# Performance work log

Hardware: AMD Instinct MI355X
Metric: run time of the kernel (lower is better)

## Reference

```python
import jax, jax.numpy as jnp
import numpy as np

K = 3; PAD = 1; STRIDE = 1; EPS = 1e-5


def setup_inputs() -> dict:
    key = jax.random.key(0)
    k0, k1, k2 = jax.random.split(key, 3)
    B, C, H, W, O = 4, 256, 64, 64, 256
    x = jax.random.normal(k0, (B, C, H, W), jnp.float32)
    # offset conv: small random weights so offsets are nontrivial but bounded
    w_off = jax.random.normal(k1, (2 * K * K, C, K, K), jnp.float32) * 0.01
    b_off = jnp.zeros((2 * K * K,), jnp.float32)
    # kaiming normal, mode=fan_out: std = sqrt(2 / (O*K*K))
    w_def = jax.random.normal(k2, (O, C, K, K), jnp.float32) * np.float32(np.sqrt(2.0 / (O * K * K)))
    gamma = jnp.ones((O,), jnp.float32)
    beta = jnp.zeros((O,), jnp.float32)
    return {"x": x, "w_off": w_off, "b_off": b_off, "w_def": w_def, "gamma": gamma, "beta": beta}


def _bilinear_gather(x, py, px):
    """x: [B,C,H,W]; py,px: [B,K2,Ho,Wo] float sample coords.
    Returns [B,K2,Ho,Wo,C] with zero padding outside (per-corner masking,
    matching torchvision deform_conv2d)."""
    B, C, H, W = x.shape
    y0f = jnp.floor(py); x0f = jnp.floor(px)
    wy1 = py - y0f; wy0 = 1.0 - wy1
    wx1 = px - x0f; wx0 = 1.0 - wx1
    bidx = jnp.arange(B)[:, None, None, None]

    def corner(yf, xf, wgt):
        valid = (yf >= 0) & (yf <= H - 1) & (xf >= 0) & (xf <= W - 1)
        yc = jnp.clip(yf.astype(jnp.int32), 0, H - 1)
        xc = jnp.clip(xf.astype(jnp.int32), 0, W - 1)
        v = x[bidx, :, yc, xc]  # [B,K2,Ho,Wo,C] (advanced idx moves C last)
        return v * (wgt * valid)[..., None]

    return (corner(y0f, x0f, wy0 * wx0) + corner(y0f, x0f + 1.0, wy0 * wx1)
            + corner(y0f + 1.0, x0f, wy1 * wx0) + corner(y0f + 1.0, x0f + 1.0, wy1 * wx1))


def _forward(x, w_off, b_off, w_def, gamma, beta):
    B, C, H, W = x.shape
    O = w_def.shape[0]
    K2 = K * K
    # 1) offset-predicting conv
    off = jax.lax.conv_general_dilated(x, w_off, (STRIDE, STRIDE), ((PAD, PAD), (PAD, PAD)))
    off = off + b_off[None, :, None, None]
    Ho, Wo = off.shape[2], off.shape[3]
    off = off.reshape(B, K2, 2, Ho, Wo)  # pairs (dy, dx) per kernel tap
    # 2) deformable sampling locations
    ky, kx = jnp.meshgrid(jnp.arange(K, dtype=jnp.float32), jnp.arange(K, dtype=jnp.float32), indexing='ij')
    base_y = (jnp.arange(Ho, dtype=jnp.float32) * STRIDE - PAD)
    base_x = (jnp.arange(Wo, dtype=jnp.float32) * STRIDE - PAD)
    py = off[:, :, 0] + ky.reshape(K2)[None, :, None, None] + base_y[None, None, :, None]
    px = off[:, :, 1] + kx.reshape(K2)[None, :, None, None] + base_x[None, None, None, :]
    vals = _bilinear_gather(x, py, px)  # [B,K2,Ho,Wo,C]
    # 3) deform conv GEMM (bias=False)
    out = jnp.einsum('bkhwc,ock->bohw', vals, w_def.reshape(O, C, K2))
    # 4) BatchNorm (training mode: batch stats) + ReLU
    mean = out.mean(axis=(0, 2, 3))
    var = out.var(axis=(0, 2, 3))
    out = (out - mean[None, :, None, None]) * (gamma * jax.lax.rsqrt(var + EPS))[None, :, None, None]
    out = out + beta[None, :, None, None]
    return jax.nn.relu(out)


def reference(x, w_off, b_off, w_def, gamma, beta):
    return _forward(x, w_off, b_off, w_def, gamma, beta)
```

## Files before the change

### kernel.cpp

```cpp
#include <hip/hip_runtime.h>
#include <hip/hip_bf16.h>

typedef unsigned int  uint;
typedef unsigned short ushort;
typedef short bf16x8 __attribute__((ext_vector_type(8)));
typedef float f32x4  __attribute__((ext_vector_type(4)));

#define HW   4096
#define KD   2304

__device__ __forceinline__ void load_lds16(const void* g, void* l) {
    __builtin_amdgcn_global_load_lds((const __attribute__((address_space(1))) void*)g,
                                     (__attribute__((address_space(3))) void*)l, 16, 0, 0);
}
__device__ __forceinline__ float blo(uint u) { return __uint_as_float(u << 16); }
__device__ __forceinline__ float bhi(uint u) { return __uint_as_float(u & 0xffff0000u); }
__device__ __forceinline__ uint pack2(float e, float o) {
    __hip_bfloat16 he = __float2bfloat16(e), ho = __float2bfloat16(o);
    return (uint)(*(ushort*)&he) | ((uint)(*(ushort*)&ho) << 16);
}

__global__ __launch_bounds__(256) void prep_all(const float* __restrict__ x,
                                                const float* __restrict__ w_def,
                                                const float* __restrict__ w_off,
                                                uint* __restrict__ x2t,
                                                ushort* __restrict__ bt,
                                                ushort* __restrict__ bt0,
                                                float* __restrict__ stats) {
    __shared__ uint tl[32][65];
    int bid = blockIdx.x;
    int t = threadIdx.x;
    if (bid < 1024) {
        int ab  = bid & 63;
        int cpb = (bid >> 6) & 3;
        int b   = bid >> 8;
#pragma unroll
        for (int i = 0; i < 8; ++i) {
            int idx = i * 256 + t;
            int cp = idx >> 6, a = idx & 63;
            const float* p = x + ((size_t)(b * 256 + (cpb * 32 + cp) * 2)) * HW + ab * 64 + a;
            tl[cp][a] = pack2(p[0], p[HW]);
        }
        __syncthreads();
#pragma unroll
        for (int i = 0; i < 8; ++i) {
            int idx = i * 256 + t;
            int a = idx >> 5, cp = idx & 31;
            x2t[((size_t)b * 4096 + ab * 64 + a) * 128 + cpb * 32 + cp] = tl[cp][a];
        }
    } else if (bid < 3328) {
        int idx = (bid - 1024) * 256 + t;
        int c   = idx & 255;
        int tap = (idx >> 8) % 9;
        int o   = idx / KD;
        __hip_bfloat16 h = __float2bfloat16(w_def[(o * 256 + c) * 9 + tap]);
        bt[idx] = *(ushort*)&h;
    } else if (bid < 3616) {
        int idx = (bid - 3328) * 256 + t;
        int c   = idx & 255;
        int tap = (idx >> 8) % 9;
        int j   = idx / KD;
        float v = (j < 18) ? w_off[(j * 256 + c) * 9 + tap] : 0.f;
        __hip_bfloat16 h = __float2bfloat16(v);
        bt0[idx] = *(ushort*)&h;
    } else {
        float4 z = {0.f, 0.f, 0.f, 0.f};
        ((float4*)stats)[t] = z;
    }
}

__global__ __attribute__((amdgpu_waves_per_eu(4, 4))) __launch_bounds__(1024)
void fused_main(const uint* __restrict__ x2t,
                const ushort* __restrict__ bt,
                const ushort* __restrict__ bt0,
                const float* __restrict__ b_off,
                float* __restrict__ out,
                float* __restrict__ stats) {
    int id = blockIdx.x;
    int xcd = id & 7;
    int b = xcd >> 1, h = (xcd & 1) * 32 + (id >> 3);
    int t = threadIdx.x;
    int wv = t >> 6, lane = t & 63;
    int mrow = lane & 15, quad = lane >> 4;
    bool producer = (wv < 8);
    int ppos = (wv << 3) + (lane >> 3);
    int pc8  = lane & 7;
    int wvc  = wv - 8;

    __shared__ __align__(16) char smem[66048];
    uint*   lX   = (uint*)smem;
    ushort* lB0  = (ushort*)(smem + 24576);
    float*  sOff = (float*)(smem + 61440);
    int*    sAc  = (int*)smem;
    float*  sWc  = (float*)(smem + 9216);
    ushort* lA   = (ushort*)(smem + 18432);

    {
        f32x4 accO = {0.f, 0.f, 0.f, 0.f};
        int mq = wv & 3, nn = (wv >> 2) & 1;
        for (int cb = 0; cb < 4; ++cb) {
#pragma unroll
            for (int s = 0; s < 2; ++s) {
                int q = s * 16 + wv;
                if (q < 24) {
                    int dy  = q >> 3;
                    int y   = h + dy - 1;
                    int sub = q & 7;
                    int wl  = sub * 8 + (lane >> 3);
                    int cps = ((lane & 7) ^ ((lane >> 3) & 7)) * 4;
                    if ((unsigned)y < 64u) {
                        const uint* src = x2t + ((size_t)(b * 4096 + y * 64 + wl)) * 128 + cb * 32 + cps;
                        load_lds16(src, &lX[q * 256]);
                    } else {
                        uint4 z = {0u, 0u, 0u, 0u};
                        *(uint4*)&lX[q * 256 + lane * 4] = z;
                    }
                }
            }
#pragma unroll
            for (int s = 0; s < 3; ++s) {
                int q = s * 16 + wv;
                if (q < 36) {
                    int e = q * 512 + lane * 8;
                    int o  = e / 576;
                    int r  = e - o * 576;
                    int chp = r >> 3;
                    int ch  = chp ^ (o & 7);
                    int tap = ch >> 3, k8 = ch & 7;
                    const ushort* src = bt0 + (size_t)o * KD + tap * 256 + cb * 64 + k8 * 8;
                    load_lds16(src, &lB0[q * 512]);
                }
            }
            __syncthreads();
            if (producer) {
#pragma unroll
                for (int tap = 0; tap < 9; ++tap) {
                    int dy = tap / 3, dx = tap % 3;
                    int xx = mq * 16 + mrow + dx - 1;
                    bool vx = (unsigned)xx < 64u;
                    int xc = min(max(xx, 0), 63);
#pragma unroll
                    for (int kb = 0; kb < 2; ++kb) {
                        int cp0 = kb * 16 + quad * 4;
                        uint4 ad = {0u, 0u, 0u, 0u};
                        if (vx) ad = *(const uint4*)&lX[dy * 2048 + xc * 32 + (cp0 ^ ((xc & 7) * 4))];
                        bf16x8 af = *(bf16x8*)&ad;
                        int o = nn * 16 + mrow;
                        int chs = (tap * 8 + (((kb * 4 + quad)) ^ (o & 7)));
                        bf16x8 bfr = *(const bf16x8*)&lB0[o * 576 + chs * 8];
                        accO = __builtin_amdgcn_mfma_f32_16x16x32_bf16(af, bfr, accO, 0, 0, 0);
                    }
                }
            }
            __syncthreads();
        }
        if (producer) {
            int o = nn * 16 + mrow;
            if (o < 18) {
                float bias = b_off[o];
                int wpos = mq * 16 + quad * 4;
                sOff[o * 64 + wpos + 0] = accO.x + bias;
                sOff[o * 64 + wpos + 1] = accO.y + bias;
                sOff[o * 64 + wpos + 2] = accO.z + bias;
                sOff[o * 64 + wpos + 3] = accO.w + bias;
            }
        }
        __syncthreads();
    }

    for (int i = t; i < 576; i += 1024) {
        int tap = i >> 6, ww = i & 63;
        float oy = sOff[(2 * tap) * 64 + ww];
        float ox = sOff[(2 * tap + 1) * 64 + ww];
        float py = oy + (float)(tap / 3 + h - 1);
        float px = ox + (float)(tap % 3 + ww - 1);
        float y0f = floorf(py), x0f = floorf(px);
        float wy1 = py - y0f, wx1 = px - x0f;
        float wy0 = 1.f - wy1, wx0 = 1.f - wx1;
        bool vy0 = (y0f >= 0.f) && (y0f <= 63.f);
        bool vy1 = (y0f >= -1.f) && (y0f <= 62.f);
        bool vx0 = (x0f >= 0.f) && (x0f <= 63.f);
        bool vx1 = (x0f >= -1.f) && (x0f <= 62.f);
        int iy0 = min(max((int)y0f, 0), 63),  iy1 = min(max((int)y0f + 1, 0), 63);
        int ix0 = min(max((int)x0f, 0), 63),  ix1 = min(max((int)x0f + 1, 0), 63);
        sAc[0 * 576 + tap * 64 + ww] = iy0 * 64 + ix0;
        sAc[1 * 576 + tap * 64 + ww] = iy0 * 64 + ix1;
        sAc[2 * 576 + tap * 64 + ww] = iy1 * 64 + ix0;
        sAc[3 * 576 + tap * 64 + ww] = iy1 * 64 + ix1;
        sWc[0 * 576 + tap * 64 + ww] = wy0 * wx0 * (float)(vy0 && vx0);
        sWc[1 * 576 + tap * 64 + ww] = wy0 * wx1 * (float)(vy0 && vx1);
        sWc[2 * 576 + tap * 64 + ww] = wy1 * wx0 * (float)(vy1 && vx0);
        sWc[3 * 576 + tap * 64 + ww] = wy1 * wx1 * (float)(vy1 && vx1);
    }
    __syncthreads();

    f32x4 acc[4][2];
#pragma unroll
    for (int m = 0; m < 4; ++m)
#pragma unroll
        for (int n = 0; n < 2; ++n) acc[m][n] = {0.f, 0.f, 0.f, 0.f};

    const uint* xb = x2t + (size_t)b * 4096 * 128;

    auto issue_gathers = [&](int sl, uint4 (&g)[4]) {
        int tap = sl >> 2, cb = sl & 3;
        const uint* xp = xb + cb * 32 + pc8 * 4;
        g[0] = *(const uint4*)(xp + (size_t)sAc[0 * 576 + tap * 64 + ppos] * 128);
        g[1] = *(const uint4*)(xp + (size_t)sAc[1 * 576 + tap * 64 + ppos] * 128);
        g[2] = *(const uint4*)(xp + (size_t)sAc[2 * 576 + tap * 64 + ppos] * 128);
        g[3] = *(const uint4*)(xp + (size_t)sAc[3 * 576 + tap * 64 + ppos] * 128);
    };
    auto finish = [&](int sl, ushort* lAb, const uint4 (&g)[4]) {
        int tap = sl >> 2;
        float f0 = sWc[0 * 576 + tap * 64 + ppos], f1 = sWc[1 * 576 + tap * 64 + ppos];
        float f2 = sWc[2 * 576 + tap * 64 + ppos], f3 = sWc[3 * 576 + tap * 64 + ppos];
        const uint* c0 = (const uint*)&g[0];
        const uint* c1 = (const uint*)&g[1];
        const uint* c2 = (const uint*)&g[2];
        const uint* c3 = (const uint*)&g[3];
        uint r[4];
#pragma unroll
        for (int j = 0; j < 4; ++j) {
            float ev = f0 * blo(c0[j]) + f1 * blo(c1[j]) + f2 * blo(c2[j]) + f3 * blo(c3[j]);
            float ov = f0 * bhi(c0[j]) + f1 * bhi(c1[j]) + f2 * bhi(c2[j]) + f3 * bhi(c3[j]);
            r[j] = pack2(ev, ov);
        }
        uint4 gg = {r[0], r[1], r[2], r[3]};
        *(uint4*)&lAb[ppos * 64 + ((pc8 ^ (ppos & 7)) * 8)] = gg;
    };
    auto loadB = [&](int sl, bf16x8 (&br)[4]) {
        int tap = sl >> 2, cb = sl & 3;
        const ushort* base = bt + tap * 256 + cb * 64 + quad * 8;
#pragma unroll
        for (int kb = 0; kb < 2; ++kb)
#pragma unroll
            for (int n = 0; n < 2; ++n) {
                int r = wvc * 32 + n * 16 + mrow;
                br[kb * 2 + n] = *(const bf16x8*)(base + (size_t)r * KD + kb * 32);
            }
    };
    auto mfma_pass = [&](int bi, const bf16x8 (&br)[4]) {
#pragma unroll
        for (int kb = 0; kb < 2; ++kb) {
            bf16x8 af[4];
#pragma unroll
            for (int m = 0; m < 4; ++m) {
                int r = m * 16 + mrow;
                af[m] = *(const bf16x8*)&lA[bi * 4096 + r * 64 + (((kb * 4 + quad) ^ (r & 7)) * 8)];
            }
#pragma unroll
            for (int n = 0; n < 2; ++n)
#pragma unroll
                for (int m = 0; m < 4; ++m)
                    acc[m][n] = __builtin_amdgcn_mfma_f32_16x16x32_bf16(af[m], br[kb * 2 + n], acc[m][n], 0, 0, 0);
        }
    };

    uint4 gA[4];
    bf16x8 brA[4], brB[4];
    if (producer) {
        issue_gathers(0, gA);
        finish(0, &lA[0], gA);
        issue_gathers(1, gA);
        finish(1, &lA[4096], gA);
        asm volatile("s_waitcnt lgkmcnt(0)" ::: "memory");
    } else {
        loadB(0, brA);
        loadB(1, brB);
    }
    __builtin_amdgcn_s_barrier();
    __builtin_amdgcn_sched_barrier(0);

    for (int s = 0; s < 36; s += 2) {
        if (producer) {
            if (s + 2 < 36) {
                issue_gathers(s + 2, gA);
                finish(s + 2, &lA[((s + 2) & 3) * 4096], gA);
                issue_gathers(s + 3, gA);
                finish(s + 3, &lA[((s + 3) & 3) * 4096], gA);
                asm volatile("s_waitcnt lgkmcnt(0)" ::: "memory");
            }
        } else {
            __builtin_amdgcn_s_setprio(1);
            mfma_pass(s & 3, brA);
            mfma_pass((s + 1) & 3, brB);
            __builtin_amdgcn_s_setprio(0);
            if (s + 2 < 36) loadB(s + 2, brA);
            if (s + 3 < 36) loadB(s + 3, brB);
        }
        __builtin_amdgcn_s_barrier();
        __builtin_amdgcn_sched_barrier(0);
    }

    if (!producer) {
#pragma unroll
        for (int n = 0; n < 2; ++n) {
            int o = wvc * 32 + n * 16 + mrow;
            float ss = 0.f, qq = 0.f;
#pragma unroll
            for (int m = 0; m < 4; ++m) {
                int pos = m * 16 + quad * 4;
                f32x4 v = acc[m][n];
                *(f32x4*)(out + ((size_t)(b * 256 + o)) * HW + h * 64 + pos) = v;
                ss += v.x + v.y + v.z + v.w;
                qq += v.x * v.x + v.y * v.y + v.z * v.z + v.w * v.w;
            }
            ss += __shfl_xor(ss, 16); ss += __shfl_xor(ss, 32);
            qq += __shfl_xor(qq, 16); qq += __shfl_xor(qq, 32);
            if (quad == 0) {
                atomicAdd(&stats[o], ss);
                atomicAdd(&stats[512 + o], qq);
            }
        }
    }
}

__global__ __launch_bounds__(256) void bn_apply(float* __restrict__ out,
                                                const float* __restrict__ stats,
                                                const float* __restrict__ gamma,
                                                const float* __restrict__ beta) {
    int bid = blockIdx.x;
    int o = (bid >> 2) & 255;
    float S = stats[o], S2 = stats[512 + o];
    float mu  = S * (1.f / 16384.f);
    float var = S2 * (1.f / 16384.f) - mu * mu;
    float sc  = gamma[o] * rsqrtf(var + 1e-5f);
    float be  = beta[o];
    int idx4 = bid * 256 + threadIdx.x;
    float4 v = ((const float4*)out)[idx4];
    v.x = fmaxf((v.x - mu) * sc + be, 0.f);
    v.y = fmaxf((v.y - mu) * sc + be, 0.f);
    v.z = fmaxf((v.z - mu) * sc + be, 0.f);
    v.w = fmaxf((v.w - mu) * sc + be, 0.f);
    ((float4*)out)[idx4] = v;
}

extern "C" void kernel_launch(void* const* d_in, const int* in_sizes, int n_in,
                              void* d_out, int out_size, void* d_ws, size_t ws_size,
                              hipStream_t stream) {
    const float* x     = (const float*)d_in[0];
    const float* w_off = (const float*)d_in[1];
    const float* b_off = (const float*)d_in[2];
    const float* w_def = (const float*)d_in[3];
    const float* gamma = (const float*)d_in[4];
    const float* beta  = (const float*)d_in[5];
    float* out = (float*)d_out;

    char* ws = (char*)d_ws;
    uint*   x2t   = (uint*)ws;
    ushort* bt    = (ushort*)(ws + 8388608);
    ushort* bt0   = (ushort*)(ws + 9568256);
    float*  stats = (float*)(ws + 9715712);

    prep_all  <<<3617, 256, 0, stream>>>(x, w_def, w_off, x2t, bt, bt0, stats);
    fused_main<<<256, 1024, 0, stream>>>(x2t, bt, bt0, b_off, out, stats);
    bn_apply  <<<4096, 256, 0, stream>>>(out, stats, gamma, beta);
}
```

Measured before the change: 144.6 us.

## Fuse prep, main GEMM and BatchNorm into one cooperative kernel with grid syncs

Merges the three launches into a single cooperative kernel. The prep stage (x transpose to bf16, weight conversion, stats zeroing) now runs inside the kernel, followed by a grid-wide sync. After the stats atomics a second grid sync lets each block apply BN and ReLU directly to its register accumulators before storing. This drops two launch gaps and the full write/read/write round-trip of the output through bn_apply. The costs are two grid barriers and a prep phase limited to 256 blocks, and the kernel depends on all 256 blocks being co-resident.

```diff
diff --git a/kernel.cpp b/kernel.cpp
--- a/kernel.cpp
+++ b/kernel.cpp
@@ -1,5 +1,6 @@
 #include <hip/hip_runtime.h>
 #include <hip/hip_bf16.h>
+#include <hip/hip_cooperative_groups.h>
 
 typedef unsigned int  uint;
 typedef unsigned short ushort;
@@ -20,70 +21,25 @@
     return (uint)(*(ushort*)&he) | ((uint)(*(ushort*)&ho) << 16);
 }
 
-__global__ __launch_bounds__(256) void prep_all(const float* __restrict__ x,
-                                                const float* __restrict__ w_def,
-                                                const float* __restrict__ w_off,
-                                                uint* __restrict__ x2t,
-                                                ushort* __restrict__ bt,
-                                                ushort* __restrict__ bt0,
-                                                float* __restrict__ stats) {
-    __shared__ uint tl[32][65];
+__global__ __attribute__((amdgpu_waves_per_eu(4, 4))) __launch_bounds__(1024)
+void mega(const float* __restrict__ x,
+          const float* __restrict__ w_def,
+          const float* __restrict__ w_off,
+          const float* __restrict__ b_off,
+          const float* __restrict__ gamma,
+          const float* __restrict__ beta,
+          uint* __restrict__ x2t,
+          ushort* __restrict__ bt,
+          ushort* __restrict__ bt0,
+          float* __restrict__ out,
+          float* __restrict__ stats) {
+    cooperative_groups::grid_group grid = cooperative_groups::this_grid();
     int bid = blockIdx.x;
-    int t = threadIdx.x;
-    if (bid < 1024) {
-        int ab  = bid & 63;
-        int cpb = (bid >> 6) & 3;
-        int b   = bid >> 8;
-#pragma unroll
-        for (int i = 0; i < 8; ++i) {
-            int idx = i * 256 + t;
-            int cp = idx >> 6, a = idx & 63;
-            const float* p = x + ((size_t)(b * 256 + (cpb * 32 + cp) * 2)) * HW + ab * 64 + a;
-            tl[cp][a] = pack2(p[0], p[HW]);
-        }
-        __syncthreads();
-#pragma unroll
-        for (int i = 0; i < 8; ++i) {
-            int idx = i * 256 + t;
-            int a = idx >> 5, cp = idx & 31;
-            x2t[((size_t)b * 4096 + ab * 64 + a) * 128 + cpb * 32 + cp] = tl[cp][a];
-        }
-    } else if (bid < 3328) {
-        int idx = (bid - 1024) * 256 + t;
-        int c   = idx & 255;
-        int tap = (idx >> 8) % 9;
-        int o   = idx / KD;
-        __hip_bfloat16 h = __float2bfloat16(w_def[(o * 256 + c) * 9 + tap]);
-        bt[idx] = *(ushort*)&h;
-    } else if (bid < 3616) {
-        int idx = (bid - 3328) * 256 + t;
-        int c   = idx & 255;
-        int tap = (idx >> 8) % 9;
-        int j   = idx / KD;
-        float v = (j < 18) ? w_off[(j * 256 + c) * 9 + tap] : 0.f;
-        __hip_bfloat16 h = __float2bfloat16(v);
-        bt0[idx] = *(ushort*)&h;
-    } else {
-        float4 z = {0.f, 0.f, 0.f, 0.f};
-        ((float4*)stats)[t] = z;
-    }
-}
-
-__global__ __attribute__((amdgpu_waves_per_eu(4, 4))) __launch_bounds__(1024)
-void fused_main(const uint* __restrict__ x2t,
-                const ushort* __restrict__ bt,
-                const ushort* __restrict__ bt0,
-                const float* __restrict__ b_off,
-                float* __restrict__ out,
-                float* __restrict__ stats) {
-    int id = blockIdx.x;
-    int xcd = id & 7;
-    int b = xcd >> 1, h = (xcd & 1) * 32 + (id >> 3);
     int t = threadIdx.x;
     int wv = t >> 6, lane = t & 63;
     int mrow = lane & 15, quad = lane >> 4;
     bool producer = (wv < 8);
-    int ppos = (wv << 3) + (lane >> 3);
+    int ppos = ((wv & 7) << 3) + (lane >> 3);
     int pc8  = lane & 7;
     int wvc  = wv - 8;
 
@@ -94,6 +50,53 @@
     int*    sAc  = (int*)smem;
     float*  sWc  = (float*)(smem + 9216);
     ushort* lA   = (ushort*)(smem + 18432);
+    uint*   tl4  = (uint*)smem;
+
+    {
+        int k = t >> 8, tsub = t & 255;
+        int tile = bid * 4 + k;
+        int ab  = tile & 63;
+        int cpb = (tile >> 6) & 3;
+        int b0  = tile >> 8;
+        uint* tl = tl4 + k * (32 * 65);
+#pragma unroll
+        for (int i = 0; i < 8; ++i) {
+            int idx = i * 256 + tsub;
+            int cp = idx >> 6, a = idx & 63;
+            const float* p = x + ((size_t)(b0 * 256 + (cpb * 32 + cp) * 2)) * HW + ab * 64 + a;
+            tl[cp * 65 + a] = pack2(p[0], p[HW]);
+        }
+        __syncthreads();
+#pragma unroll
+        for (int i = 0; i < 8; ++i) {
+            int idx = i * 256 + tsub;
+            int a = idx >> 5, cp = idx & 31;
+            x2t[((size_t)b0 * 4096 + ab * 64 + a) * 128 + cpb * 32 + cp] = tl[cp * 65 + a];
+        }
+        for (int idx = bid * 1024 + t; idx < 589824; idx += 262144) {
+            int c   = idx & 255;
+            int tap = (idx >> 8) % 9;
+            int o   = idx / KD;
+            __hip_bfloat16 hh = __float2bfloat16(w_def[(o * 256 + c) * 9 + tap]);
+            bt[idx] = *(ushort*)&hh;
+        }
+        {
+            int idx = bid * 1024 + t;
+            if (idx < 73728) {
+                int c   = idx & 255;
+                int tap = (idx >> 8) % 9;
+                int j   = idx / KD;
+                float v = (j < 18) ? w_off[(j * 256 + c) * 9 + tap] : 0.f;
+                __hip_bfloat16 hh = __float2bfloat16(v);
+                bt0[idx] = *(ushort*)&hh;
+            }
+        }
+        if (bid == 0) stats[t] = 0.f;
+    }
+    grid.sync();
+
+    int xcd = bid & 7;
+    int b = xcd >> 1, h = (xcd & 1) * 32 + (bid >> 3);
 
     {
         f32x4 accO = {0.f, 0.f, 0.f, 0.f};
@@ -155,10 +158,10 @@
             __syncthreads();
         }
         if (producer) {
-            int o = nn * 16 + mrow;
+            int o = (wv >> 2 & 1) * 16 + mrow;
             if (o < 18) {
                 float bias = b_off[o];
-                int wpos = mq * 16 + quad * 4;
+                int wpos = (wv & 3) * 16 + quad * 4;
                 sOff[o * 64 + wpos + 0] = accO.x + bias;
                 sOff[o * 64 + wpos + 1] = accO.y + bias;
                 sOff[o * 64 + wpos + 2] = accO.z + bias;
@@ -299,9 +302,7 @@
             float ss = 0.f, qq = 0.f;
 #pragma unroll
             for (int m = 0; m < 4; ++m) {
-                int pos = m * 16 + quad * 4;
                 f32x4 v = acc[m][n];
-                *(f32x4*)(out + ((size_t)(b * 256 + o)) * HW + h * 64 + pos) = v;
                 ss += v.x + v.y + v.z + v.w;
                 qq += v.x * v.x + v.y * v.y + v.z * v.z + v.w * v.w;
             }
@@ -313,26 +314,30 @@
             }
         }
     }
-}
-
-__global__ __launch_bounds__(256) void bn_apply(float* __restrict__ out,
-                                                const float* __restrict__ stats,
-                                                const float* __restrict__ gamma,
-                                                const float* __restrict__ beta) {
-    int bid = blockIdx.x;
-    int o = (bid >> 2) & 255;
-    float S = stats[o], S2 = stats[512 + o];
-    float mu  = S * (1.f / 16384.f);
-    float var = S2 * (1.f / 16384.f) - mu * mu;
-    float sc  = gamma[o] * rsqrtf(var + 1e-5f);
-    float be  = beta[o];
-    int idx4 = bid * 256 + threadIdx.x;
-    float4 v = ((const float4*)out)[idx4];
-    v.x = fmaxf((v.x - mu) * sc + be, 0.f);
-    v.y = fmaxf((v.y - mu) * sc + be, 0.f);
-    v.z = fmaxf((v.z - mu) * sc + be, 0.f);
-    v.w = fmaxf((v.w - mu) * sc + be, 0.f);
-    ((float4*)out)[idx4] = v;
+    grid.sync();
+
+    if (!producer) {
+#pragma unroll
+        for (int n = 0; n < 2; ++n) {
+            int o = wvc * 32 + n * 16 + mrow;
+            float S  = __hip_atomic_load(&stats[o],       __ATOMIC_RELAXED, __HIP_MEMORY_SCOPE_AGENT);
+            float S2 = __hip_atomic_load(&stats[512 + o], __ATOMIC_RELAXED, __HIP_MEMORY_SCOPE_AGENT);
+            float mu  = S * (1.f / 16384.f);
+            float var = S2 * (1.f / 16384.f) - mu * mu;
+            float sc  = gamma[o] * rsqrtf(var + 1e-5f);
+            float be  = beta[o];
+#pragma unroll
+            for (int m = 0; m < 4; ++m) {
+                int pos = m * 16 + quad * 4;
+                f32x4 v = acc[m][n];
+                v.x = fmaxf((v.x - mu) * sc + be, 0.f);
+                v.y = fmaxf((v.y - mu) * sc + be, 0.f);
+                v.z = fmaxf((v.z - mu) * sc + be, 0.f);
+                v.w = fmaxf((v.w - mu) * sc + be, 0.f);
+                *(f32x4*)(out + ((size_t)(b * 256 + o)) * HW + h * 64 + pos) = v;
+            }
+        }
+    }
 }
 
 extern "C" void kernel_launch(void* const* d_in, const int* in_sizes, int n_in,
@@ -352,7 +357,9 @@
     ushort* bt0   = (ushort*)(ws + 9568256);
     float*  stats = (float*)(ws + 9715712);
 
-    prep_all  <<<3617, 256, 0, stream>>>(x, w_def, w_off, x2t, bt, bt0, stats);
-    fused_main<<<256, 1024, 0, stream>>>(x2t, bt, bt0, b_off, out, stats);
-    bn_apply  <<<4096, 256, 0, stream>>>(out, stats, gamma, beta);
+    void* args[] = {(void*)&x, (void*)&w_def, (void*)&w_off, (void*)&b_off,
+                    (void*)&gamma, (void*)&beta, (void*)&x2t, (void*)&bt,
+                    (void*)&bt0, (void*)&out, (void*)&stats};
+    hipLaunchCooperativeKernel((const void*)mega, dim3(256), dim3(1024),
+                               args, 0, stream);
 }
```

After: 203.1 us. 1.4x slower.

## Fuse BatchNorm apply into main kernel via grid-wide atomic barrier

Applied to the files above, without the earlier changes.

Removes the separate bn_apply launch. After the GEMM and the partial stat atomics, every block increments a global counter and spins until all 256 blocks have arrived. It then reads the final statistics and writes normalized, ReLU'd outputs straight from the accumulators. This avoids writing the 16MB output and then reading and writing it again, and saves one launch. The cost is a grid-wide spin barrier, which assumes all 256 blocks are co-resident, and a counter reset that relies on prep_all zeroing the stats slot.

```diff
diff --git a/kernel.cpp b/kernel.cpp
--- a/kernel.cpp
+++ b/kernel.cpp
@@ -74,6 +74,8 @@
                 const ushort* __restrict__ bt,
                 const ushort* __restrict__ bt0,
                 const float* __restrict__ b_off,
+                const float* __restrict__ gamma,
+                const float* __restrict__ beta,
                 float* __restrict__ out,
                 float* __restrict__ stats) {
     int id = blockIdx.x;
@@ -83,7 +85,7 @@
     int wv = t >> 6, lane = t & 63;
     int mrow = lane & 15, quad = lane >> 4;
     bool producer = (wv < 8);
-    int ppos = (wv << 3) + (lane >> 3);
+    int ppos = ((wv & 7) << 3) + (lane >> 3);
     int pc8  = lane & 7;
     int wvc  = wv - 8;
 
@@ -155,10 +157,10 @@
             __syncthreads();
         }
         if (producer) {
-            int o = nn * 16 + mrow;
+            int o = ((wv >> 2) & 1) * 16 + mrow;
             if (o < 18) {
                 float bias = b_off[o];
-                int wpos = mq * 16 + quad * 4;
+                int wpos = (wv & 3) * 16 + quad * 4;
                 sOff[o * 64 + wpos + 0] = accO.x + bias;
                 sOff[o * 64 + wpos + 1] = accO.y + bias;
                 sOff[o * 64 + wpos + 2] = accO.z + bias;
@@ -299,9 +301,7 @@
             float ss = 0.f, qq = 0.f;
 #pragma unroll
             for (int m = 0; m < 4; ++m) {
-                int pos = m * 16 + quad * 4;
                 f32x4 v = acc[m][n];
-                *(f32x4*)(out + ((size_t)(b * 256 + o)) * HW + h * 64 + pos) = v;
                 ss += v.x + v.y + v.z + v.w;
                 qq += v.x * v.x + v.y * v.y + v.z * v.z + v.w * v.w;
             }
@@ -313,26 +313,40 @@
             }
         }
     }
-}
-
-__global__ __launch_bounds__(256) void bn_apply(float* __restrict__ out,
-                                                const float* __restrict__ stats,
-                                                const float* __restrict__ gamma,
-                                                const float* __restrict__ beta) {
-    int bid = blockIdx.x;
-    int o = (bid >> 2) & 255;
-    float S = stats[o], S2 = stats[512 + o];
-    float mu  = S * (1.f / 16384.f);
-    float var = S2 * (1.f / 16384.f) - mu * mu;
-    float sc  = gamma[o] * rsqrtf(var + 1e-5f);
-    float be  = beta[o];
-    int idx4 = bid * 256 + threadIdx.x;
-    float4 v = ((const float4*)out)[idx4];
-    v.x = fmaxf((v.x - mu) * sc + be, 0.f);
-    v.y = fmaxf((v.y - mu) * sc + be, 0.f);
-    v.z = fmaxf((v.z - mu) * sc + be, 0.f);
-    v.w = fmaxf((v.w - mu) * sc + be, 0.f);
-    ((float4*)out)[idx4] = v;
+    __syncthreads();
+
+    if (t == 0) {
+        __threadfence();
+        uint* cnt = (uint*)&stats[1023];
+        __hip_atomic_fetch_add(cnt, 1u, __ATOMIC_ACQ_REL, __HIP_MEMORY_SCOPE_AGENT);
+        while (__hip_atomic_load(cnt, __ATOMIC_ACQUIRE, __HIP_MEMORY_SCOPE_AGENT) < 256u) {
+            __builtin_amdgcn_s_sleep(2);
+        }
+    }
+    __syncthreads();
+
+    if (!producer) {
+#pragma unroll
+        for (int n = 0; n < 2; ++n) {
+            int o = wvc * 32 + n * 16 + mrow;
+            float S  = __hip_atomic_load(&stats[o],       __ATOMIC_RELAXED, __HIP_MEMORY_SCOPE_AGENT);
+            float S2 = __hip_atomic_load(&stats[512 + o], __ATOMIC_RELAXED, __HIP_MEMORY_SCOPE_AGENT);
+            float mu  = S * (1.f / 16384.f);
+            float var = S2 * (1.f / 16384.f) - mu * mu;
+            float sc  = gamma[o] * rsqrtf(var + 1e-5f);
+            float be  = beta[o];
+#pragma unroll
+            for (int m = 0; m < 4; ++m) {
+                int pos = m * 16 + quad * 4;
+                f32x4 v = acc[m][n];
+                v.x = fmaxf((v.x - mu) * sc + be, 0.f);
+                v.y = fmaxf((v.y - mu) * sc + be, 0.f);
+                v.z = fmaxf((v.z - mu) * sc + be, 0.f);
+                v.w = fmaxf((v.w - mu) * sc + be, 0.f);
+                *(f32x4*)(out + ((size_t)(b * 256 + o)) * HW + h * 64 + pos) = v;
+            }
+        }
+    }
 }
 
 extern "C" void kernel_launch(void* const* d_in, const int* in_sizes, int n_in,
@@ -353,6 +367,5 @@
     float*  stats = (float*)(ws + 9715712);
 
     prep_all  <<<3617, 256, 0, stream>>>(x, w_def, w_off, x2t, bt, bt0, stats);
-    fused_main<<<256, 1024, 0, stream>>>(x2t, bt, bt0, b_off, out, stats);
-    bn_apply  <<<4096, 256, 0, stream>>>(out, stats, gamma, beta);
-}
+    fused_main<<<256, 1024, 0, stream>>>(x2t, bt, bt0, b_off, gamma, beta, out, stats);
+}
```

Result: slower. 155.8 us (+7.8%).

## Split output channels across two blocks per row to double grid size

Applied to the files above, without the earlier changes.

Doubles the fused kernel grid so each block handles one half of the 256 output channels for a given (batch, row), with each consumer wave computing 16 channels instead of 32. This is meant to raise occupancy across CUs, since 256 blocks of 1024 threads underfill the device. The cost is that each half-block redoes the offset conv and the bilinear gather/interpolation of A, doubling that producer work and its gather traffic.

```diff
diff --git a/kernel.cpp b/kernel.cpp
--- a/kernel.cpp
+++ b/kernel.cpp
@@ -77,13 +77,15 @@
                 float* __restrict__ out,
                 float* __restrict__ stats) {
     int id = blockIdx.x;
-    int xcd = id & 7;
-    int b = xcd >> 1, h = (xcd & 1) * 32 + (id >> 3);
+    int nh = id & 1;
+    int bid2 = id >> 1;
+    int xcd = bid2 & 7;
+    int b = xcd >> 1, h = (xcd & 1) * 32 + (bid2 >> 3);
     int t = threadIdx.x;
     int wv = t >> 6, lane = t & 63;
     int mrow = lane & 15, quad = lane >> 4;
     bool producer = (wv < 8);
-    int ppos = (wv << 3) + (lane >> 3);
+    int ppos = ((wv & 7) << 3) + (lane >> 3);
     int pc8  = lane & 7;
     int wvc  = wv - 8;
 
@@ -155,10 +157,10 @@
             __syncthreads();
         }
         if (producer) {
-            int o = nn * 16 + mrow;
+            int o = ((wv >> 2) & 1) * 16 + mrow;
             if (o < 18) {
                 float bias = b_off[o];
-                int wpos = mq * 16 + quad * 4;
+                int wpos = (wv & 3) * 16 + quad * 4;
                 sOff[o * 64 + wpos + 0] = accO.x + bias;
                 sOff[o * 64 + wpos + 1] = accO.y + bias;
                 sOff[o * 64 + wpos + 2] = accO.z + bias;
@@ -194,11 +196,9 @@
     }
     __syncthreads();
 
-    f32x4 acc[4][2];
-#pragma unroll
-    for (int m = 0; m < 4; ++m)
-#pragma unroll
-        for (int n = 0; n < 2; ++n) acc[m][n] = {0.f, 0.f, 0.f, 0.f};
+    f32x4 acc[4];
+#pragma unroll
+    for (int m = 0; m < 4; ++m) acc[m] = {0.f, 0.f, 0.f, 0.f};
 
     const uint* xb = x2t + (size_t)b * 4096 * 128;
 
@@ -228,18 +228,14 @@
         uint4 gg = {r[0], r[1], r[2], r[3]};
         *(uint4*)&lAb[ppos * 64 + ((pc8 ^ (ppos & 7)) * 8)] = gg;
     };
-    auto loadB = [&](int sl, bf16x8 (&br)[4]) {
+    auto loadB = [&](int sl, bf16x8 (&br)[2]) {
         int tap = sl >> 2, cb = sl & 3;
-        const ushort* base = bt + tap * 256 + cb * 64 + quad * 8;
-#pragma unroll
-        for (int kb = 0; kb < 2; ++kb)
-#pragma unroll
-            for (int n = 0; n < 2; ++n) {
-                int r = wvc * 32 + n * 16 + mrow;
-                br[kb * 2 + n] = *(const bf16x8*)(base + (size_t)r * KD + kb * 32);
-            }
+        int r = nh * 128 + wvc * 16 + mrow;
+        const ushort* base = bt + (size_t)r * KD + tap * 256 + cb * 64 + quad * 8;
+        br[0] = *(const bf16x8*)(base);
+        br[1] = *(const bf16x8*)(base + 32);
     };
-    auto mfma_pass = [&](int bi, const bf16x8 (&br)[4]) {
+    auto mfma_pass = [&](int bi, const bf16x8 (&br)[2]) {
 #pragma unroll
         for (int kb = 0; kb < 2; ++kb) {
             bf16x8 af[4];
@@ -249,15 +245,13 @@
                 af[m] = *(const bf16x8*)&lA[bi * 4096 + r * 64 + (((kb * 4 + quad) ^ (r & 7)) * 8)];
             }
 #pragma unroll
-            for (int n = 0; n < 2; ++n)
-#pragma unroll
-                for (int m = 0; m < 4; ++m)
-                    acc[m][n] = __builtin_amdgcn_mfma_f32_16x16x32_bf16(af[m], br[kb * 2 + n], acc[m][n], 0, 0, 0);
+            for (int m = 0; m < 4; ++m)
+                acc[m] = __builtin_amdgcn_mfma_f32_16x16x32_bf16(af[m], br[kb], acc[m], 0, 0, 0);
         }
     };
 
     uint4 gA[4];
-    bf16x8 brA[4], brB[4];
+    bf16x8 brA[2], brB[2];
     if (producer) {
         issue_gathers(0, gA);
         finish(0, &lA[0], gA);
@@ -293,24 +287,21 @@
     }
 
     if (!producer) {
-#pragma unroll
-        for (int n = 0; n < 2; ++n) {
-            int o = wvc * 32 + n * 16 + mrow;
-            float ss = 0.f, qq = 0.f;
-#pragma unroll
-            for (int m = 0; m < 4; ++m) {
-                int pos = m * 16 + quad * 4;
-                f32x4 v = acc[m][n];
-                *(f32x4*)(out + ((size_t)(b * 256 + o)) * HW + h * 64 + pos) = v;
-                ss += v.x + v.y + v.z + v.w;
-                qq += v.x * v.x + v.y * v.y + v.z * v.z + v.w * v.w;
-            }
-            ss += __shfl_xor(ss, 16); ss += __shfl_xor(ss, 32);
-            qq += __shfl_xor(qq, 16); qq += __shfl_xor(qq, 32);
-            if (quad == 0) {
-                atomicAdd(&stats[o], ss);
-                atomicAdd(&stats[512 + o], qq);
-            }
+        int o = nh * 128 + wvc * 16 + mrow;
+        float ss = 0.f, qq = 0.f;
+#pragma unroll
+        for (int m = 0; m < 4; ++m) {
+            int pos = m * 16 + quad * 4;
+            f32x4 v = acc[m];
+            *(f32x4*)(out + ((size_t)(b * 256 + o)) * HW + h * 64 + pos) = v;
+            ss += v.x + v.y + v.z + v.w;
+            qq += v.x * v.x + v.y * v.y + v.z * v.z + v.w * v.w;
+        }
+        ss += __shfl_xor(ss, 16); ss += __shfl_xor(ss, 32);
+        qq += __shfl_xor(qq, 16); qq += __shfl_xor(qq, 32);
+        if (quad == 0) {
+            atomicAdd(&stats[o], ss);
+            atomicAdd(&stats[512 + o], qq);
         }
     }
 }
@@ -353,6 +344,6 @@
     float*  stats = (float*)(ws + 9715712);
 
     prep_all  <<<3617, 256, 0, stream>>>(x, w_def, w_off, x2t, bt, bt0, stats);
-    fused_main<<<256, 1024, 0, stream>>>(x2t, bt, bt0, b_off, out, stats);
+    fused_main<<<512, 1024, 0, stream>>>(x2t, bt, bt0, b_off, out, stats);
     bn_apply  <<<4096, 256, 0, stream>>>(out, stats, gamma, beta);
 }
```

Result: slower. 168.5 us (+16.6%).
